# Kernel optimization log

Measured on AMD Instinct MI355X. Metric: run time of the kernel, lower is better.

## Reference

```python
import jax, jax.numpy as jnp
import numpy as np

EMBED_DIM = 256
HIDDEN_DIM = 128
NUM_VARS = 1024


def _linear_params(key, fan_in, fan_out):
    kw, kb = jax.random.split(key)
    lim = 1.0 / np.sqrt(fan_in)
    W = jax.random.uniform(kw, (fan_in, fan_out), minval=-lim, maxval=lim, dtype=jnp.float32)
    b = jax.random.uniform(kb, (fan_out,), minval=-lim, maxval=lim, dtype=jnp.float32)
    return W, b


def setup_inputs() -> dict:
    key = jax.random.key(0)
    ks = jax.random.split(key, 7)
    next_state_embedding = jax.random.normal(ks[0], (EMBED_DIM,), dtype=jnp.float32)
    prev_variable_embeddings = jax.random.normal(ks[1], (NUM_VARS, EMBED_DIM), dtype=jnp.float32)
    Wq, bq = _linear_params(ks[2], EMBED_DIM, HIDDEN_DIM)
    Wk, bk = _linear_params(ks[3], EMBED_DIM, HIDDEN_DIM)
    Wc, bc = _linear_params(ks[4], EMBED_DIM, HIDDEN_DIM)
    W1, b1 = _linear_params(ks[5], 2 * HIDDEN_DIM, HIDDEN_DIM)
    W2, b2 = _linear_params(ks[6], HIDDEN_DIM, 1)
    return {
        "next_state_embedding": next_state_embedding,
        "prev_variable_embeddings": prev_variable_embeddings,
        "Wq": Wq, "bq": bq,
        "Wk": Wk, "bk": bk,
        "Wc": Wc, "bc": bc,
        "W1": W1, "b1": b1,
        "W2": W2, "b2": b2,
    }


def reference(next_state_embedding, prev_variable_embeddings,
              Wq, bq, Wk, bk, Wc, bc, W1, b1, W2, b2):
    n = prev_variable_embeddings.shape[0]
    h = Wq.shape[1]
    # context_net: Linear + ReLU on next-state embedding -> [h]
    context = jax.nn.relu(next_state_embedding @ Wc + bc)
    # queries/keys over prev vars, each shifted by context -> [n, h]
    queries = prev_variable_embeddings @ Wq + bq + context
    keys = prev_variable_embeddings @ Wk + bk + context
    # pair_scorer layer 1 on concat(q_i, k_j) decomposes:
    # hidden[i,j] = relu(q_i @ W1[:h] + k_j @ W1[h:] + b1)
    q_proj = queries @ W1[:h]            # [n, h]
    k_proj = keys @ W1[h:]               # [n, h]
    hidden = jax.nn.relu(q_proj[:, None, :] + k_proj[None, :, :] + b1)  # [n, n, h]
    scores = jnp.squeeze(hidden @ W2, axis=-1) + b2[0]  # [n, n]
    # extract i < j pairs in row-major order (matches the nested loop)
    iu, ju = jnp.triu_indices(n, k=1)
    return scores[iu, ju]  # [n*(n-1)/2]
```

## Files before the change

kernel.cpp:

```cpp
#include <hip/hip_runtime.h>

#define N 1024
#define E 256
#define H 128

typedef _Float16 hv2 __attribute__((ext_vector_type(2)));
typedef _Float16 half_t;

__device__ __forceinline__ float dot2_acc(hv2 a, hv2 b, float c) {
#if __has_builtin(__builtin_amdgcn_fdot2)
    return __builtin_amdgcn_fdot2(a, b, c, false);
#else
    return c + (float)a.x * (float)b.x + (float)a.y * (float)b.y;
#endif
}

__device__ __forceinline__ hv2 relu_add2(hv2 a, hv2 b) {
    hv2 s = a + b;
    hv2 z = (hv2)(_Float16)0.f;
    return __builtin_elementwise_max(s, z);
}

__global__ __launch_bounds__(256) void setup_kernel(
    const float* __restrict__ x, const float* __restrict__ Wc, const float* __restrict__ bc,
    const float* __restrict__ Wq, const float* __restrict__ bq,
    const float* __restrict__ Wk, const float* __restrict__ bk,
    const float* __restrict__ W1, const float* __restrict__ b1,
    float* __restrict__ Wqp, float* __restrict__ Wkp,
    float* __restrict__ constq, float* __restrict__ constk) {
    int b = blockIdx.x;
    int t = threadIdx.x;
    if (b < E) {
        __shared__ float wq_s[H], wk_s[H];
        if (t < H) wq_s[t] = Wq[b * H + t];
        else       wk_s[t - H] = Wk[b * H + (t - H)];
        __syncthreads();
        int h = t & (H - 1);
        float acc = 0.f;
        if (t < H) {
#pragma unroll 8
            for (int r = 0; r < H; ++r) acc += wq_s[r] * W1[r * H + h];
            Wqp[b * H + h] = acc;
        } else {
#pragma unroll 8
            for (int r = 0; r < H; ++r) acc += wk_s[r] * W1[(H + r) * H + h];
            Wkp[b * H + h] = acc;
        }
    } else {
        __shared__ float xs[E];
        __shared__ float pc[2][H];
        __shared__ float aq_s[H], ak_s[H];
        xs[t] = x[t];
        __syncthreads();
        int h = t & (H - 1);
        int c = t >> 7;
        float p = 0.f;
#pragma unroll 8
        for (int e = c * H; e < c * H + H; ++e) p += xs[e] * Wc[e * H + h];
        pc[c][h] = p;
        __syncthreads();
        if (t < H) {
            float ctxv = fmaxf(pc[0][t] + pc[1][t] + bc[t], 0.f);
            aq_s[t] = bq[t] + ctxv;
            ak_s[t] = bk[t] + ctxv;
        }
        __syncthreads();
        float acc;
        if (t < H) {
            acc = b1[h];
#pragma unroll 8
            for (int r = 0; r < H; ++r) acc += aq_s[r] * W1[r * H + h];
            constq[h] = acc;
        } else {
            acc = 0.f;
#pragma unroll 8
            for (int r = 0; r < H; ++r) acc += ak_s[r] * W1[(H + r) * H + h];
            constk[h] = acc;
        }
    }
}

__global__ __launch_bounds__(256) void proj_kernel(
    const float* __restrict__ P,
    const float* __restrict__ Wqp, const float* __restrict__ Wkp,
    const float* __restrict__ constq, const float* __restrict__ constk,
    half_t* __restrict__ qh, half_t* __restrict__ kh) {
    __shared__ __align__(16) float p_s[4 * E];
    int b = blockIdx.x;
    int i0 = b * 4;
    int t = threadIdx.x;
    ((float4*)p_s)[t] = ((const float4*)(P + i0 * E))[t];
    __syncthreads();
    bool isq = t < H;
    int h = t & (H - 1);
    const float* M = isq ? Wqp : Wkp;
    float cv = isq ? constq[h] : constk[h];
    float a0 = cv, a1 = cv, a2 = cv, a3 = cv;
    for (int e = 0; e < E; e += 4) {
        float4 p0 = *(const float4*)&p_s[0 * E + e];
        float4 p1 = *(const float4*)&p_s[1 * E + e];
        float4 p2 = *(const float4*)&p_s[2 * E + e];
        float4 p3 = *(const float4*)&p_s[3 * E + e];
        float m0 = M[(e + 0) * H + h];
        float m1 = M[(e + 1) * H + h];
        float m2 = M[(e + 2) * H + h];
        float m3 = M[(e + 3) * H + h];
        a0 += p0.x * m0 + p0.y * m1 + p0.z * m2 + p0.w * m3;
        a1 += p1.x * m0 + p1.y * m1 + p1.z * m2 + p1.w * m3;
        a2 += p2.x * m0 + p2.y * m1 + p2.z * m2 + p2.w * m3;
        a3 += p3.x * m0 + p3.y * m1 + p3.z * m2 + p3.w * m3;
    }
    half_t* O = isq ? qh : kh;
    O[(i0 + 0) * H + h] = (half_t)a0;
    O[(i0 + 1) * H + h] = (half_t)a1;
    O[(i0 + 2) * H + h] = (half_t)a2;
    O[(i0 + 3) * H + h] = (half_t)a3;
}

#define QSTR 136
#define NTILE 32
__global__ __launch_bounds__(256) void pair_kernel(
    const half_t* __restrict__ qh, const half_t* __restrict__ kh,
    const float* __restrict__ W2, const float* __restrict__ b2,
    float* __restrict__ out) {
    int tid = blockIdx.x;
    int bi = (int)((65.0f - sqrtf(4225.0f - 8.0f * (float)tid)) * 0.5f);
    while (bi > 0 && tid < 32 * bi - bi * (bi - 1) / 2) --bi;
    while (tid >= 32 * (bi + 1) - (bi + 1) * bi / 2) ++bi;
    int bj = bi + (tid - (32 * bi - bi * (bi - 1) / 2));

    __shared__ __align__(16) half_t qs[32][QSTR];
    __shared__ __align__(16) half_t ks[32][QSTR];
    __shared__ __align__(16) half_t w2s[H];

    int t = threadIdx.x;
    if (t < H) w2s[t] = (half_t)W2[t];

    const float4* qh4 = (const float4*)(qh + bi * 32 * H);
    const float4* kh4 = (const float4*)(kh + bj * 32 * H);
#pragma unroll
    for (int v = 0; v < 2; ++v) {
        int idx = v * 256 + t;
        int r = idx >> 4, c = idx & 15;
        float4 q = qh4[idx];
        float4 k = kh4[idx];
        *(float4*)&qs[r][c * 8] = q;
        *(float4*)&ks[r][c * 8] = k;
    }
    __syncthreads();

    int jj  = t & 31;
    int ti0 = t >> 5;
    float b2v = b2[0];
    float acc[4];
#pragma unroll
    for (int u = 0; u < 4; ++u) acc[u] = b2v;

    for (int h8 = 0; h8 < 16; ++h8) {
        float4 wf = *(const float4*)&w2s[h8 * 8];
        float4 kv = *(const float4*)&ks[jj][h8 * 8];
        const hv2* wp = (const hv2*)&wf;
        const hv2* kp2 = (const hv2*)&kv;
#pragma unroll
        for (int u = 0; u < 4; ++u) {
            float4 qf = *(const float4*)&qs[ti0 + u * 8][h8 * 8];
            const hv2* qp2 = (const hv2*)&qf;
#pragma unroll
            for (int s = 0; s < 4; ++s) {
                hv2 sa = relu_add2(qp2[s], kp2[s]);
                acc[u] = dot2_acc(sa, wp[s], acc[u]);
            }
        }
    }

#pragma unroll
    for (int u = 0; u < 4; ++u) {
        int i = bi * 32 + ti0 + u * 8;
        int j = bj * 32 + jj;
        if (j > i) {
            int base = i * (2 * N - i - 1) / 2;
            out[base + (j - i - 1)] = acc[u];
        }
    }
}

extern "C" void kernel_launch(void* const* d_in, const int* in_sizes, int n_in,
                              void* d_out, int out_size, void* d_ws, size_t ws_size,
                              hipStream_t stream) {
    const float* x  = (const float*)d_in[0];
    const float* P  = (const float*)d_in[1];
    const float* Wq = (const float*)d_in[2];
    const float* bq = (const float*)d_in[3];
    const float* Wk = (const float*)d_in[4];
    const float* bk = (const float*)d_in[5];
    const float* Wc = (const float*)d_in[6];
    const float* bc = (const float*)d_in[7];
    const float* W1 = (const float*)d_in[8];
    const float* b1 = (const float*)d_in[9];
    const float* W2 = (const float*)d_in[10];
    const float* b2 = (const float*)d_in[11];
    float* out = (float*)d_out;

    float* ws     = (float*)d_ws;
    float* constq = ws;
    float* constk = ws + H;
    float* Wqp    = ws + 2 * H;
    float* Wkp    = Wqp + E * H;
    half_t* qh    = (half_t*)(Wkp + E * H);
    half_t* kh    = qh + N * H;

    setup_kernel<<<E + 1, 256, 0, stream>>>(x, Wc, bc, Wq, bq, Wk, bk, W1, b1,
                                            Wqp, Wkp, constq, constk);
    proj_kernel<<<N / 4, 256, 0, stream>>>(P, Wqp, Wkp, constq, constk, qh, kh);
    pair_kernel<<<528, 256, 0, stream>>>(qh, kh, W2, b2, out);
}
```

Baseline: 102.1 us.

## Store folded projection weights as packed fp16 and use dot2 in projection

The setup kernel now computes two embedding rows per block and writes the folded Wq·W1 and Wk·W1 weights as fp16 in an interleaved hv4 layout. The projection kernel converts its P rows to fp16 and accumulates with packed fp16 dot2 instructions, which halves weight bandwidth and the instruction count. The pair kernel also keeps W2 in registers instead of rereading it from shared memory on every iteration. The cost is lower precision in the projected weights and inputs, and higher register pressure in the pair kernel.

```diff
diff --git a/kernel.cpp b/kernel.cpp
--- a/kernel.cpp
+++ b/kernel.cpp
@@ -4,8 +4,9 @@
 #define E 256
 #define H 128
 
+typedef _Float16 half_t;
 typedef _Float16 hv2 __attribute__((ext_vector_type(2)));
-typedef _Float16 half_t;
+typedef _Float16 hv4 __attribute__((ext_vector_type(4)));
 
 __device__ __forceinline__ float dot2_acc(hv2 a, hv2 b, float c) {
 #if __has_builtin(__builtin_amdgcn_fdot2)
@@ -26,26 +27,33 @@
     const float* __restrict__ Wq, const float* __restrict__ bq,
     const float* __restrict__ Wk, const float* __restrict__ bk,
     const float* __restrict__ W1, const float* __restrict__ b1,
-    float* __restrict__ Wqp, float* __restrict__ Wkp,
+    hv2* __restrict__ Wqp2, hv2* __restrict__ Wkp2,
     float* __restrict__ constq, float* __restrict__ constk) {
     int b = blockIdx.x;
     int t = threadIdx.x;
-    if (b < E) {
-        __shared__ float wq_s[H], wk_s[H];
-        if (t < H) wq_s[t] = Wq[b * H + t];
-        else       wk_s[t - H] = Wk[b * H + (t - H)];
-        __syncthreads();
-        int h = t & (H - 1);
-        float acc = 0.f;
-        if (t < H) {
-#pragma unroll 8
-            for (int r = 0; r < H; ++r) acc += wq_s[r] * W1[r * H + h];
-            Wqp[b * H + h] = acc;
-        } else {
-#pragma unroll 8
-            for (int r = 0; r < H; ++r) acc += wk_s[r] * W1[(H + r) * H + h];
-            Wkp[b * H + h] = acc;
-        }
+    if (b < E / 2) {
+        __shared__ float wq_s[2][H], wk_s[2][H];
+        {
+            int r = t >> 7, c = t & 127;
+            wq_s[r][c] = Wq[(2 * b + r) * H + c];
+            wk_s[r][c] = Wk[(2 * b + r) * H + c];
+        }
+        __syncthreads();
+        int h = t & 127;
+        bool isq = t < H;
+        const float* M = isq ? W1 : (W1 + H * H);
+        const float* w0 = isq ? wq_s[0] : wk_s[0];
+        const float* w1r = isq ? wq_s[1] : wk_s[1];
+        float a0 = 0.f, a1 = 0.f;
+#pragma unroll 4
+        for (int r = 0; r < H; ++r) {
+            float m = M[r * H + h];
+            a0 += w0[r] * m;
+            a1 += w1r[r] * m;
+        }
+        hv2 o; o.x = (half_t)a0; o.y = (half_t)a1;
+        hv2* O = isq ? Wqp2 : Wkp2;
+        O[((b >> 1) * H + h) * 2 + (b & 1)] = o;
     } else {
         __shared__ float xs[E];
         __shared__ float pc[2][H];
@@ -82,33 +90,37 @@
 
 __global__ __launch_bounds__(256) void proj_kernel(
     const float* __restrict__ P,
-    const float* __restrict__ Wqp, const float* __restrict__ Wkp,
+    const hv4* __restrict__ Wqp4, const hv4* __restrict__ Wkp4,
     const float* __restrict__ constq, const float* __restrict__ constk,
     half_t* __restrict__ qh, half_t* __restrict__ kh) {
-    __shared__ __align__(16) float p_s[4 * E];
+    __shared__ __align__(16) hv4 ps4[64][4];
     int b = blockIdx.x;
     int i0 = b * 4;
     int t = threadIdx.x;
-    ((float4*)p_s)[t] = ((const float4*)(P + i0 * E))[t];
+    {
+        int row = t >> 6, e4 = t & 63;
+        float4 v = ((const float4*)(P + (i0 + row) * E))[e4];
+        hv4 o; o.x = (half_t)v.x; o.y = (half_t)v.y; o.z = (half_t)v.z; o.w = (half_t)v.w;
+        ps4[e4][row] = o;
+    }
     __syncthreads();
     bool isq = t < H;
     int h = t & (H - 1);
-    const float* M = isq ? Wqp : Wkp;
+    const hv4* M = isq ? Wqp4 : Wkp4;
     float cv = isq ? constq[h] : constk[h];
     float a0 = cv, a1 = cv, a2 = cv, a3 = cv;
-    for (int e = 0; e < E; e += 4) {
-        float4 p0 = *(const float4*)&p_s[0 * E + e];
-        float4 p1 = *(const float4*)&p_s[1 * E + e];
-        float4 p2 = *(const float4*)&p_s[2 * E + e];
-        float4 p3 = *(const float4*)&p_s[3 * E + e];
-        float m0 = M[(e + 0) * H + h];
-        float m1 = M[(e + 1) * H + h];
-        float m2 = M[(e + 2) * H + h];
-        float m3 = M[(e + 3) * H + h];
-        a0 += p0.x * m0 + p0.y * m1 + p0.z * m2 + p0.w * m3;
-        a1 += p1.x * m0 + p1.y * m1 + p1.z * m2 + p1.w * m3;
-        a2 += p2.x * m0 + p2.y * m1 + p2.z * m2 + p2.w * m3;
-        a3 += p3.x * m0 + p3.y * m1 + p3.z * m2 + p3.w * m3;
+    for (int e4 = 0; e4 < 64; ++e4) {
+        hv4 m = M[e4 * H + h];
+        const hv2* m2 = (const hv2*)&m;
+        hv4 p0 = ps4[e4][0], p1 = ps4[e4][1], p2 = ps4[e4][2], p3 = ps4[e4][3];
+        const hv2* q0 = (const hv2*)&p0;
+        const hv2* q1 = (const hv2*)&p1;
+        const hv2* q2 = (const hv2*)&p2;
+        const hv2* q3 = (const hv2*)&p3;
+        a0 = dot2_acc(q0[0], m2[0], a0); a0 = dot2_acc(q0[1], m2[1], a0);
+        a1 = dot2_acc(q1[0], m2[0], a1); a1 = dot2_acc(q1[1], m2[1], a1);
+        a2 = dot2_acc(q2[0], m2[0], a2); a2 = dot2_acc(q2[1], m2[1], a2);
+        a3 = dot2_acc(q3[0], m2[0], a3); a3 = dot2_acc(q3[1], m2[1], a3);
     }
     half_t* O = isq ? qh : kh;
     O[(i0 + 0) * H + h] = (half_t)a0;
@@ -118,7 +130,6 @@
 }
 
 #define QSTR 136
-#define NTILE 32
 __global__ __launch_bounds__(256) void pair_kernel(
     const half_t* __restrict__ qh, const half_t* __restrict__ kh,
     const float* __restrict__ W2, const float* __restrict__ b2,
@@ -149,6 +160,10 @@
     }
     __syncthreads();
 
+    float4 wreg[16];
+#pragma unroll
+    for (int h8 = 0; h8 < 16; ++h8) wreg[h8] = *(const float4*)&w2s[h8 * 8];
+
     int jj  = t & 31;
     int ti0 = t >> 5;
     float b2v = b2[0];
@@ -157,9 +172,8 @@
     for (int u = 0; u < 4; ++u) acc[u] = b2v;
 
     for (int h8 = 0; h8 < 16; ++h8) {
-        float4 wf = *(const float4*)&w2s[h8 * 8];
         float4 kv = *(const float4*)&ks[jj][h8 * 8];
-        const hv2* wp = (const hv2*)&wf;
+        const hv2* wp = (const hv2*)&wreg[h8];
         const hv2* kp2 = (const hv2*)&kv;
 #pragma unroll
         for (int u = 0; u < 4; ++u) {
@@ -204,13 +218,13 @@
     float* ws     = (float*)d_ws;
     float* constq = ws;
     float* constk = ws + H;
-    float* Wqp    = ws + 2 * H;
-    float* Wkp    = Wqp + E * H;
-    half_t* qh    = (half_t*)(Wkp + E * H);
+    hv4* Wqp4     = (hv4*)(ws + 2 * H);
+    hv4* Wkp4     = Wqp4 + (E / 4) * H;
+    half_t* qh    = (half_t*)(Wkp4 + (E / 4) * H);
     half_t* kh    = qh + N * H;
 
-    setup_kernel<<<E + 1, 256, 0, stream>>>(x, Wc, bc, Wq, bq, Wk, bk, W1, b1,
-                                            Wqp, Wkp, constq, constk);
-    proj_kernel<<<N / 4, 256, 0, stream>>>(P, Wqp, Wkp, constq, constk, qh, kh);
+    setup_kernel<<<E / 2 + 1, 256, 0, stream>>>(x, Wc, bc, Wq, bq, Wk, bk, W1, b1,
+                                                (hv2*)Wqp4, (hv2*)Wkp4, constq, constk);
+    proj_kernel<<<N / 4, 256, 0, stream>>>(P, Wqp4, Wkp4, constq, constk, qh, kh);
     pair_kernel<<<528, 256, 0, stream>>>(qh, kh, W2, b2, out);
 }
```

Measured after the change: 103.7 us. About the same (+1.5%).
